# Performance work log

Measured on AMD Instinct MI355X. Metric: run time of the kernel, lower is better.

The kernel has to match this reference:

```python
import jax, jax.numpy as jnp
import numpy as np

DIM = 512; NH = 8; AG = 144; WIN = 18; PS = 12; B = 128; N0 = 320


def _pool_matrix(in_size, out_size):
    # PyTorch AdaptiveAvgPool2d window rule: start=floor(i*in/out), end=ceil((i+1)*in/out)
    P = np.zeros((out_size, in_size), np.float32)
    for i in range(out_size):
        s = (i * in_size) // out_size
        e = -((-(i + 1) * in_size) // out_size)
        P[i, s:e] = 1.0 / (e - s)
    return jnp.asarray(P)


def setup_inputs() -> dict:
    key = jax.random.key(0)
    ks = jax.random.split(key, 12)
    std = 0.02
    return {
        "x": jax.random.normal(ks[0], (B, N0, DIM), jnp.float32),
        "qkv_w": jax.random.normal(ks[1], (DIM, 3 * DIM), jnp.float32) * 0.02,
        "proj_w": jax.random.normal(ks[2], (DIM, DIM), jnp.float32) * 0.02,
        "proj_b": jnp.zeros((DIM,), jnp.float32),
        "dwc_w": jax.random.normal(ks[3], (DIM, 1, 3, 3), jnp.float32) * 0.1,
        "dwc_b": jnp.zeros((DIM,), jnp.float32),
        "an_bias": jax.random.normal(ks[4], (NH, AG, 7, 7), jnp.float32) * std,
        "na_bias": jax.random.normal(ks[5], (NH, AG, 7, 7), jnp.float32) * std,
        "ah_bias": jax.random.normal(ks[6], (1, NH, AG, WIN, 1), jnp.float32) * std,
        "aw_bias": jax.random.normal(ks[7], (1, NH, AG, 1, WIN), jnp.float32) * std,
        "ha_bias": jax.random.normal(ks[8], (1, NH, WIN, 1, AG), jnp.float32) * std,
        "wa_bias": jax.random.normal(ks[9], (1, NH, 1, WIN, AG), jnp.float32) * std,
    }


def reference(x, qkv_w, proj_w, proj_b, dwc_w, dwc_b,
              an_bias, na_bias, ah_bias, aw_bias, ha_bias, wa_bias):
    b, n0, c = x.shape
    x1 = jnp.pad(x, ((0, 0), (2, 2), (0, 0)))          # pad 2 tokens each side
    n = n0 + 4
    h = w = int(n ** 0.5)
    hd = c // NH
    scale = hd ** -0.5

    qkv = x1 @ qkv_w                                    # (b, n, 3c), no bias
    q, k, v = jnp.split(qkv, 3, axis=-1)

    # agent tokens: adaptive avg pool of q on the (h, w) grid to (PS, PS)
    P = _pool_matrix(h, PS)                             # (12, 18)
    qg = q.reshape(b, h, w, c)
    agent = jnp.einsum('oh,bhwc,pw->bopc', P, qg, P).reshape(b, AG, c)

    def heads(t):
        return t.reshape(b, n, NH, hd).transpose(0, 2, 1, 3)
    q, k, v = heads(q), heads(k), heads(v)              # (b, H, n, hd)
    ag = agent.reshape(b, AG, NH, hd).transpose(0, 2, 1, 3)  # (b, H, A, hd)

    # stage 1: agent <- keys  (ac_bias is concatenated then sliced off => no-op)
    pb1 = jax.image.resize(an_bias, (NH, AG, WIN, WIN), 'bilinear').reshape(1, NH, AG, WIN * WIN)
    pb2 = (ah_bias + aw_bias).reshape(1, NH, AG, WIN * WIN)
    agent_attn = jax.nn.softmax(
        jnp.einsum('bhad,bhnd->bhan', ag * scale, k) + pb1 + pb2, axis=-1)
    agent_v = jnp.einsum('bhan,bhnd->bhad', agent_attn, v)   # (b, H, A, hd)

    # stage 2: queries <- agents (ca_bias sliced off => no-op)
    ab1 = jax.image.resize(na_bias, (NH, AG, WIN, WIN), 'bilinear') \
        .reshape(1, NH, AG, WIN * WIN).transpose(0, 1, 3, 2)  # (1, H, n, A)
    ab2 = (ha_bias + wa_bias).reshape(1, NH, WIN * WIN, AG)
    q_attn = jax.nn.softmax(
        jnp.einsum('bhnd,bhad->bhna', q * scale, ag) + ab1 + ab2, axis=-1)
    out = jnp.einsum('bhna,bhad->bhnd', q_attn, agent_v)
    out = out.transpose(0, 2, 1, 3).reshape(b, n, c)

    # depthwise conv skip on v
    vimg = v.transpose(0, 2, 1, 3).reshape(b, h, w, c).transpose(0, 3, 1, 2)  # (b, c, h, w)
    dwc = jax.lax.conv_general_dilated(vimg, dwc_w, (1, 1), 'SAME',
                                       feature_group_count=c)
    dwc = dwc + dwc_b[None, :, None, None]
    out = out + dwc.transpose(0, 2, 3, 1).reshape(b, n, c)

    out = out @ proj_w + proj_b
    return out[:, 2:-2, :]
```

## Files before the change

kernel.cpp:

```cpp
#include <hip/hip_runtime.h>

typedef unsigned short u16;
typedef short bf16x8 __attribute__((ext_vector_type(8)));
typedef float f32x4 __attribute__((ext_vector_type(4)));

#define B_    128
#define N0_   320
#define C_    512
#define NH_   8
#define HD_   64
#define NTOK  324
#define H_    18
#define AG_   144
#define SCALE 0.125f

typedef __attribute__((address_space(3))) unsigned int as3_u32;
typedef __attribute__((address_space(1))) const unsigned int as1_u32;

__device__ __forceinline__ void gl_lds16(const void* g, void* l) {
  __builtin_amdgcn_global_load_lds((as1_u32*)(unsigned long long)g,
                                   (as3_u32*)(unsigned int)(unsigned long long)l,
                                   16, 0, 0);
}

__device__ __forceinline__ float bfu2f(u16 u) {
  union { unsigned int u; float f; } v; v.u = ((unsigned int)u) << 16; return v.f;
}
__device__ __forceinline__ u16 f2bfu(float f) {
  union { float f; unsigned int u; } v; v.f = f;
  unsigned int r = v.u + 0x7fffu + ((v.u >> 16) & 1u);
  return (u16)(r >> 16);
}

__global__ __launch_bounds__(256) void conv_x(const float* __restrict__ x, u16* __restrict__ xp)
{
  const int idx = blockIdx.x * 256 + threadIdx.x;
  const int row = idx >> 6, c8 = idx & 63;
  const int b = row / NTOK, t = row - b * NTOK;
  u16 o[8];
  if (t < 2 || t >= 322) {
    #pragma unroll
    for (int j = 0; j < 8; ++j) o[j] = 0;
  } else {
    const float* src = x + ((size_t)(b * N0_ + (t - 2))) * C_ + c8 * 8;
    const float4 f0 = *(const float4*)(src);
    const float4 f1 = *(const float4*)(src + 4);
    o[0]=f2bfu(f0.x); o[1]=f2bfu(f0.y); o[2]=f2bfu(f0.z); o[3]=f2bfu(f0.w);
    o[4]=f2bfu(f1.x); o[5]=f2bfu(f1.y); o[6]=f2bfu(f1.z); o[7]=f2bfu(f1.w);
  }
  *(bf16x8*)&xp[(size_t)row * C_ + c8 * 8] = *(bf16x8*)o;
}

__global__ __launch_bounds__(256) void tconv(const float* __restrict__ W, u16* __restrict__ Wt, int ncols)
{
  __shared__ float T[64][65];
  const int k0 = blockIdx.x * 64, n0 = blockIdx.y * 64;
  const int tid = threadIdx.x;
  const int rr = tid >> 4, cc = tid & 15;
  #pragma unroll
  for (int i = 0; i < 4; ++i) {
    const float4 f = *(const float4*)&W[(size_t)(k0 + i * 16 + rr) * ncols + n0 + cc * 4];
    T[i * 16 + rr][cc * 4 + 0] = f.x; T[i * 16 + rr][cc * 4 + 1] = f.y;
    T[i * 16 + rr][cc * 4 + 2] = f.z; T[i * 16 + rr][cc * 4 + 3] = f.w;
  }
  __syncthreads();
  #pragma unroll
  for (int i = 0; i < 4; ++i) {
    const int n = i * 16 + rr;
    ushort4 u;
    u.x = f2bfu(T[cc * 4 + 0][n]); u.y = f2bfu(T[cc * 4 + 1][n]);
    u.z = f2bfu(T[cc * 4 + 2][n]); u.w = f2bfu(T[cc * 4 + 3][n]);
    *(ushort4*)&Wt[(size_t)(n0 + n) * 512 + k0 + cc * 4] = u;
  }
}

template<int MODE>
__global__ __launch_bounds__(256) void mfma_gemm(
    const u16* __restrict__ A, const u16* __restrict__ Bt,
    u16* __restrict__ qb, u16* __restrict__ kb, u16* __restrict__ vb,
    const float* __restrict__ bias, float* __restrict__ outf)
{
  __shared__ __align__(16) u16 As[128 * 64];
  __shared__ __align__(16) u16 Bs[128 * 64];
  const int bx = blockIdx.x;
  const int by = blockIdx.y;
  const int tid = threadIdx.x;
  const int wv = tid >> 6, lane = tid & 63;
  const int lr = lane & 15, lk = lane >> 4;
  const int wr = wv >> 1, wc = wv & 1;
  const int si = lane >> 3, slot = lane & 7;

  size_t arow_src[4];
  #pragma unroll
  for (int jj = 0; jj < 4; ++jj) {
    const int rl = (wv * 4 + jj) * 8 + si;
    const int r = by * 128 + rl;
    if (MODE == 0) {
      arow_src[jj] = (size_t)r * 512;
    } else {
      const int b2 = r / N0_, ii = r - b2 * N0_;
      arow_src[jj] = ((size_t)b2 * 8 * NTOK + (ii + 2)) * 64;
    }
  }

  f32x4 acc[4][4] = {};
  for (int k0 = 0; k0 < 512; k0 += 64) {
    __syncthreads();
    #pragma unroll
    for (int jj = 0; jj < 4; ++jj) {
      const int rl = (wv * 4 + jj) * 8 + si;
      const int c = slot ^ (rl & 7);
      const u16* asrc = (MODE == 0)
          ? (A + arow_src[jj] + k0 + c * 8)
          : (A + arow_src[jj] + (size_t)(k0 >> 6) * (NTOK * 64) + c * 8);
      gl_lds16(asrc, (char*)As + (wv * 4 + jj) * 1024);
      gl_lds16(Bt + (size_t)(bx * 128 + rl) * 512 + k0 + c * 8,
               (char*)Bs + (wv * 4 + jj) * 1024);
    }
    __syncthreads();
    #pragma unroll
    for (int kk = 0; kk < 2; ++kk) {
      bf16x8 af[4], bf[4];
      #pragma unroll
      for (int m = 0; m < 4; ++m) {
        const int row = wr * 64 + m * 16 + lr;
        af[m] = *(const bf16x8*)((const char*)As + row * 128 + (((kk * 4 + lk) ^ (row & 7)) << 4));
      }
      #pragma unroll
      for (int n = 0; n < 4; ++n) {
        const int row = wc * 64 + n * 16 + lr;
        bf[n] = *(const bf16x8*)((const char*)Bs + row * 128 + (((kk * 4 + lk) ^ (row & 7)) << 4));
      }
      #pragma unroll
      for (int m = 0; m < 4; ++m)
        #pragma unroll
        for (int n = 0; n < 4; ++n)
          acc[m][n] = __builtin_amdgcn_mfma_f32_16x16x32_bf16(af[m], bf[n], acc[m][n], 0, 0, 0);
    }
  }

  if (MODE == 0) {
    const int mat = (bx * 128) >> 9;
    u16* outp = (mat == 0) ? qb : (mat == 1) ? kb : vb;
    #pragma unroll
    for (int m = 0; m < 4; ++m) {
      #pragma unroll
      for (int r = 0; r < 4; ++r) {
        const int row = by * 128 + wr * 64 + m * 16 + lk * 4 + r;
        const int b = row / NTOK, t = row - b * NTOK;
        #pragma unroll
        for (int n = 0; n < 4; ++n) {
          const int col = bx * 128 + wc * 64 + n * 16 + lr;
          const int rem = col & 511, h = rem >> 6, d = rem & 63;
          outp[(((size_t)(b * NH_ + h)) * NTOK + t) * HD_ + d] = f2bfu(acc[m][n][r]);
        }
      }
    }
  } else {
    #pragma unroll
    for (int m = 0; m < 4; ++m) {
      #pragma unroll
      for (int r = 0; r < 4; ++r) {
        const int row = by * 128 + wr * 64 + m * 16 + lk * 4 + r;
        #pragma unroll
        for (int n = 0; n < 4; ++n) {
          const int col = bx * 128 + wc * 64 + n * 16 + lr;
          outf[(size_t)row * C_ + col] = acc[m][n][r] + bias[col];
        }
      }
    }
  }
}

__global__ void bias_kernel(const float* __restrict__ an, const float* __restrict__ na,
                            const float* __restrict__ ah, const float* __restrict__ aw,
                            const float* __restrict__ ha, const float* __restrict__ wa,
                            float* __restrict__ bAN, float* __restrict__ bNA)
{
  const int blk = blockIdx.x;
  const int h = blk / AG_, a = blk - h * AG_;
  const int tid = threadIdx.x;
  if (tid >= NTOK) return;
  const int y = tid / H_, x = tid - y * H_;
  float cy = (y + 0.5f) * (7.0f / 18.0f) - 0.5f; cy = fminf(fmaxf(cy, 0.f), 6.f);
  float cx = (x + 0.5f) * (7.0f / 18.0f) - 0.5f; cx = fminf(fmaxf(cx, 0.f), 6.f);
  const int y0 = (int)floorf(cy); const float ty = cy - y0; const int y1 = min(y0 + 1, 6);
  const int x0 = (int)floorf(cx); const float tx = cx - x0; const int x1 = min(x0 + 1, 6);
  const float w00 = (1.f - ty) * (1.f - tx), w01 = (1.f - ty) * tx;
  const float w10 = ty * (1.f - tx), w11 = ty * tx;
  const float* anp = an + (size_t)blk * 49;
  const float* nap = na + (size_t)blk * 49;
  const float van = w00 * anp[y0*7+x0] + w01 * anp[y0*7+x1] + w10 * anp[y1*7+x0] + w11 * anp[y1*7+x1];
  const float vna = w00 * nap[y0*7+x0] + w01 * nap[y0*7+x1] + w10 * nap[y1*7+x0] + w11 * nap[y1*7+x1];
  bAN[(size_t)blk * NTOK + tid] = van + ah[(size_t)blk * H_ + y] + aw[(size_t)blk * H_ + x];
  bNA[((size_t)h * NTOK + tid) * AG_ + a] =
      vna + ha[((size_t)h * H_ + y) * AG_ + a] + wa[((size_t)h * H_ + x) * AG_ + a];
}

__global__ __launch_bounds__(512) void pool_kernel(const u16* __restrict__ qb, u16* __restrict__ agb)
{
  const int blk = blockIdx.x;
  const int b = blk / AG_, a = blk - b * AG_;
  const int o = a / 12, pc = a - o * 12;
  const int y0 = (3 * o) >> 1, x0 = (3 * pc) >> 1;
  const int c = threadIdx.x; const int h = c >> 6, d = c & 63;
  const size_t base = ((size_t)(b * NH_ + h)) * NTOK * HD_ + d;
  const int t00 = (y0 * H_ + x0) * HD_;
  const float v = bfu2f(qb[base + t00]) + bfu2f(qb[base + t00 + HD_])
                + bfu2f(qb[base + t00 + H_ * HD_]) + bfu2f(qb[base + t00 + H_ * HD_ + HD_]);
  agb[((size_t)(b * NH_ + h)) * AG_ * HD_ + a * HD_ + d] = f2bfu(0.25f * v);
}

__global__ __launch_bounds__(576) void fused_attn(
    const u16* __restrict__ kb, const u16* __restrict__ vb,
    const u16* __restrict__ qb, const u16* __restrict__ agb,
    const float* __restrict__ bAN, const float* __restrict__ bNA,
    const float* __restrict__ dwc_w, const float* __restrict__ dwc_b,
    u16* __restrict__ aob)
{
  __shared__ __align__(16) u16 vT[64 * 360];
  __shared__ __align__(16) u16 avT[64 * 168];
  __shared__ __align__(16) u16 pW[9][16][40];
  const int bh = blockIdx.x, h = bh & 7;
  const int tid = threadIdx.x;
  const int mt = tid >> 6;
  const int l = tid & 63, lr = l & 15, lk = l >> 4;

  for (int idx = tid; idx < 128; idx += 576)
    *(bf16x8*)&avT[(idx >> 1) * 168 + 144 + (idx & 1) * 8] = (bf16x8){0,0,0,0,0,0,0,0};

  const u16* vsrc = vb + (size_t)bh * NTOK * HD_;
  for (int idx = tid; idx < 64 * 45; idx += 576) {
    const int d = idx & 63, c = idx >> 6;
    bf16x8 tv;
    #pragma unroll
    for (int j = 0; j < 8; ++j) {
      const int n = c * 8 + j;
      tv[j] = (n < NTOK) ? (short)vsrc[(size_t)n * HD_ + d] : (short)0;
    }
    *(bf16x8*)&vT[d * 360 + c * 8] = tv;
  }

  const u16* aga = agb + ((size_t)bh * AG_ + mt * 16 + lr) * HD_ + lk * 8;
  const bf16x8 a0 = *(const bf16x8*)(aga);
  const bf16x8 a1 = *(const bf16x8*)(aga + 32);

  f32x4 acc[21];
  const u16* kbase = kb + (size_t)bh * NTOK * HD_ + lk * 8;
  #pragma unroll
  for (int nt = 0; nt < 21; ++nt) {
    const bf16x8 b0 = *(const bf16x8*)(kbase + (size_t)(nt * 16 + lr) * HD_);
    const bf16x8 b1 = *(const bf16x8*)(kbase + (size_t)(nt * 16 + lr) * HD_ + 32);
    f32x4 c = {0.f, 0.f, 0.f, 0.f};
    c = __builtin_amdgcn_mfma_f32_16x16x32_bf16(a0, b0, c, 0, 0, 0);
    c = __builtin_amdgcn_mfma_f32_16x16x32_bf16(a1, b1, c, 0, 0, 0);
    acc[nt] = c;
  }

  const float* bb = bAN + ((size_t)h * AG_ + mt * 16) * NTOK;
  float mx[4] = {-1e30f, -1e30f, -1e30f, -1e30f};
  #pragma unroll
  for (int nt = 0; nt < 21; ++nt) {
    const int col = nt * 16 + lr;
    const bool valid = (nt < 20) || (lr < 4);
    #pragma unroll
    for (int r = 0; r < 4; ++r) {
      float s = -1e30f;
      if (valid) s = acc[nt][r] * SCALE + bb[(lk * 4 + r) * NTOK + col];
      acc[nt][r] = s;
      mx[r] = fmaxf(mx[r], s);
    }
  }
  #pragma unroll
  for (int r = 0; r < 4; ++r) {
    #pragma unroll
    for (int o = 1; o < 16; o <<= 1) mx[r] = fmaxf(mx[r], __shfl_xor(mx[r], o));
  }
  float sm[4] = {0.f, 0.f, 0.f, 0.f};
  #pragma unroll
  for (int nt = 0; nt < 21; ++nt) {
    #pragma unroll
    for (int r = 0; r < 4; ++r) {
      const float e = __expf(acc[nt][r] - mx[r]);
      acc[nt][r] = e;
      sm[r] += e;
    }
  }
  #pragma unroll
  for (int r = 0; r < 4; ++r) {
    #pragma unroll
    for (int o = 1; o < 16; o <<= 1) sm[r] += __shfl_xor(sm[r], o);
    sm[r] = 1.0f / sm[r];
  }

  __syncthreads();

  f32x4 ov[4];
  #pragma unroll
  for (int nt2 = 0; nt2 < 4; ++nt2) ov[nt2] = (f32x4){0.f, 0.f, 0.f, 0.f};
  for (int ks = 0; ks < 11; ++ks) {
    #pragma unroll
    for (int half = 0; half < 2; ++half) {
      const int nt = 2 * ks + half;
      #pragma unroll
      for (int r = 0; r < 4; ++r)
        pW[mt][lk * 4 + r][half * 16 + lr] = (nt < 21) ? f2bfu(acc[nt][r] * sm[r]) : (u16)0;
    }
    const bf16x8 pa = *(const bf16x8*)&pW[mt][lr][lk * 8];
    #pragma unroll
    for (int nt2 = 0; nt2 < 4; ++nt2) {
      const bf16x8 vf = *(const bf16x8*)&vT[(nt2 * 16 + lr) * 360 + ks * 32 + lk * 8];
      ov[nt2] = __builtin_amdgcn_mfma_f32_16x16x32_bf16(pa, vf, ov[nt2], 0, 0, 0);
    }
  }
  #pragma unroll
  for (int nt2 = 0; nt2 < 4; ++nt2) {
    ushort4 u;
    u.x = f2bfu(ov[nt2][0]); u.y = f2bfu(ov[nt2][1]);
    u.z = f2bfu(ov[nt2][2]); u.w = f2bfu(ov[nt2][3]);
    *(ushort4*)&avT[(nt2 * 16 + lr) * 168 + mt * 16 + lk * 4] = u;
  }

  __syncthreads();

  u16* aout = aob + (size_t)bh * NTOK * HD_;
  for (int mt2 = mt; mt2 < 21; mt2 += 9) {
    const int arow = min(mt2 * 16 + lr, NTOK - 1);
    const u16* qa = qb + ((size_t)bh * NTOK + arow) * HD_ + lk * 8;
    const bf16x8 qa0 = *(const bf16x8*)(qa);
    const bf16x8 qa1 = *(const bf16x8*)(qa + 32);

    f32x4 acc2[9];
    #pragma unroll
    for (int nt = 0; nt < 9; ++nt) {
      const u16* bp = agb + ((size_t)bh * AG_ + nt * 16 + lr) * HD_ + lk * 8;
      f32x4 c = {0.f, 0.f, 0.f, 0.f};
      c = __builtin_amdgcn_mfma_f32_16x16x32_bf16(qa0, *(const bf16x8*)(bp), c, 0, 0, 0);
      c = __builtin_amdgcn_mfma_f32_16x16x32_bf16(qa1, *(const bf16x8*)(bp + 32), c, 0, 0, 0);
      acc2[nt] = c;
    }

    float mx2[4] = {-1e30f, -1e30f, -1e30f, -1e30f};
    #pragma unroll
    for (int nt = 0; nt < 9; ++nt) {
      #pragma unroll
      for (int r = 0; r < 4; ++r) {
        const int trow = min(mt2 * 16 + lk * 4 + r, NTOK - 1);
        const float s = acc2[nt][r] * SCALE + bNA[((size_t)h * NTOK + trow) * AG_ + nt * 16 + lr];
        acc2[nt][r] = s;
        mx2[r] = fmaxf(mx2[r], s);
      }
    }
    #pragma unroll
    for (int r = 0; r < 4; ++r) {
      #pragma unroll
      for (int o = 1; o < 16; o <<= 1) mx2[r] = fmaxf(mx2[r], __shfl_xor(mx2[r], o));
    }
    float sm2[4] = {0.f, 0.f, 0.f, 0.f};
    #pragma unroll
    for (int nt = 0; nt < 9; ++nt) {
      #pragma unroll
      for (int r = 0; r < 4; ++r) {
        const float e = __expf(acc2[nt][r] - mx2[r]);
        acc2[nt][r] = e;
        sm2[r] += e;
      }
    }
    #pragma unroll
    for (int r = 0; r < 4; ++r) {
      #pragma unroll
      for (int o = 1; o < 16; o <<= 1) sm2[r] += __shfl_xor(sm2[r], o);
      sm2[r] = 1.0f / sm2[r];
    }

    f32x4 ov2[4];
    #pragma unroll
    for (int nt2 = 0; nt2 < 4; ++nt2) ov2[nt2] = (f32x4){0.f, 0.f, 0.f, 0.f};
    for (int ks = 0; ks < 5; ++ks) {
      #pragma unroll
      for (int half = 0; half < 2; ++half) {
        const int nt = 2 * ks + half;
        #pragma unroll
        for (int r = 0; r < 4; ++r)
          pW[mt][lk * 4 + r][half * 16 + lr] = (nt < 9) ? f2bfu(acc2[nt][r] * sm2[r]) : (u16)0;
      }
      const bf16x8 pa = *(const bf16x8*)&pW[mt][lr][lk * 8];
      #pragma unroll
      for (int nt2 = 0; nt2 < 4; ++nt2) {
        const bf16x8 vf = *(const bf16x8*)&avT[(nt2 * 16 + lr) * 168 + ks * 32 + lk * 8];
        ov2[nt2] = __builtin_amdgcn_mfma_f32_16x16x32_bf16(pa, vf, ov2[nt2], 0, 0, 0);
      }
    }

    #pragma unroll
    for (int nt2 = 0; nt2 < 4; ++nt2) {
      const int d = nt2 * 16 + lr;
      const float* wp = dwc_w + (size_t)(h * 64 + d) * 9;
      float w9[9];
      #pragma unroll
      for (int j = 0; j < 9; ++j) w9[j] = wp[j];
      const float cb = dwc_b[h * 64 + d];
      #pragma unroll
      for (int r = 0; r < 4; ++r) {
        const int t = mt2 * 16 + lk * 4 + r;
        if (t < NTOK) {
          const int y = t / H_, x = t - y * H_;
          float conv = cb;
          #pragma unroll
          for (int ky = 0; ky < 3; ++ky) {
            const int yy = y + ky - 1;
            if (yy < 0 || yy >= H_) continue;
            #pragma unroll
            for (int kx = 0; kx < 3; ++kx) {
              const int xc = x + kx - 1;
              if (xc < 0 || xc >= H_) continue;
              conv += w9[ky * 3 + kx] * bfu2f(vT[d * 360 + yy * H_ + xc]);
            }
          }
          aout[(size_t)t * HD_ + d] = f2bfu(ov2[nt2][r] + conv);
        }
      }
    }
  }
}

extern "C" void kernel_launch(void* const* d_in, const int* in_sizes, int n_in,
                              void* d_out, int out_size, void* d_ws, size_t ws_size,
                              hipStream_t stream)
{
  (void)in_sizes; (void)n_in; (void)out_size;
  const float* x      = (const float*)d_in[0];
  const float* qkv_w  = (const float*)d_in[1];
  const float* proj_w = (const float*)d_in[2];
  const float* proj_b = (const float*)d_in[3];
  const float* dwc_w  = (const float*)d_in[4];
  const float* dwc_b  = (const float*)d_in[5];
  const float* an     = (const float*)d_in[6];
  const float* na     = (const float*)d_in[7];
  const float* ah     = (const float*)d_in[8];
  const float* aw     = (const float*)d_in[9];
  const float* ha     = (const float*)d_in[10];
  const float* wa     = (const float*)d_in[11];

  char* ws = (char*)d_ws;
  const size_t QB  = (size_t)B_ * NH_ * NTOK * HD_ * 2;
  const size_t AGB = (size_t)B_ * NH_ * AG_  * HD_ * 2;
  const size_t BB  = (size_t)NH_ * AG_ * NTOK * 4;
  const size_t WQ  = (size_t)1536 * 512 * 2;
  const size_t WP  = (size_t)512 * 512 * 2;
  u16* qb    = (u16*)(ws);
  u16* kb    = (u16*)(ws + QB);
  u16* vb    = (u16*)(ws + 2 * QB);
  u16* xp    = (u16*)(ws + 3 * QB);
  u16* agb   = (u16*)(ws + 3 * QB);
  float* bAN = (float*)(ws + 3 * QB + AGB);
  float* bNA = (float*)(ws + 3 * QB + AGB + BB);
  u16* wqkvT = (u16*)(ws + 4 * QB);
  u16* wprojT= (u16*)(ws + 4 * QB + WQ);
  u16* aob   = kb;
  if (ws_size < 4 * QB + WQ + WP) return;

  conv_x   <<<dim3(B_ * NTOK * 64 / 256), dim3(256), 0, stream>>>(x, xp);
  tconv    <<<dim3(8, 24), dim3(256), 0, stream>>>(qkv_w, wqkvT, 1536);
  tconv    <<<dim3(8, 8),  dim3(256), 0, stream>>>(proj_w, wprojT, 512);
  mfma_gemm<0><<<dim3(12, 324), dim3(256), 0, stream>>>(xp, wqkvT, qb, kb, vb, nullptr, nullptr);
  pool_kernel<<<dim3(B_ * AG_),  dim3(512), 0, stream>>>(qb, agb);
  bias_kernel<<<dim3(NH_ * AG_), dim3(324), 0, stream>>>(an, na, ah, aw, ha, wa, bAN, bNA);
  fused_attn<<<dim3(B_ * NH_), dim3(576), 0, stream>>>(kb, vb, qb, agb, bAN, bNA, dwc_w, dwc_b, aob);
  mfma_gemm<1><<<dim3(4, 320), dim3(256), 0, stream>>>(aob, wprojT, nullptr, nullptr, nullptr, proj_b, (float*)d_out);
}
```

Measured before the change: 526.8 us.

## Store attention biases in bf16, stage dwc weights in LDS, vectorize output stores

Position-bias tables are stored as bf16 instead of fp32, halving the bias traffic read by the fused attention kernel. The depthwise-conv weights and bias are staged once per block into LDS as bf16 instead of being reloaded from global memory per tile. The second-stage PV MFMA swaps operands so each lane holds four consecutive channels of one token, which allows ushort4 vectorized output stores. It also wraps the MFMA loops with s_setprio, and rounding the biases and conv weights to bf16 slightly lowers accuracy.

```diff
diff --git a/kernel.cpp b/kernel.cpp
--- a/kernel.cpp
+++ b/kernel.cpp
@@ -175,7 +175,7 @@
 __global__ void bias_kernel(const float* __restrict__ an, const float* __restrict__ na,
                             const float* __restrict__ ah, const float* __restrict__ aw,
                             const float* __restrict__ ha, const float* __restrict__ wa,
-                            float* __restrict__ bAN, float* __restrict__ bNA)
+                            u16* __restrict__ bAN, u16* __restrict__ bNA)
 {
   const int blk = blockIdx.x;
   const int h = blk / AG_, a = blk - h * AG_;
@@ -192,9 +192,9 @@
   const float* nap = na + (size_t)blk * 49;
   const float van = w00 * anp[y0*7+x0] + w01 * anp[y0*7+x1] + w10 * anp[y1*7+x0] + w11 * anp[y1*7+x1];
   const float vna = w00 * nap[y0*7+x0] + w01 * nap[y0*7+x1] + w10 * nap[y1*7+x0] + w11 * nap[y1*7+x1];
-  bAN[(size_t)blk * NTOK + tid] = van + ah[(size_t)blk * H_ + y] + aw[(size_t)blk * H_ + x];
+  bAN[(size_t)blk * NTOK + tid] = f2bfu(van + ah[(size_t)blk * H_ + y] + aw[(size_t)blk * H_ + x]);
   bNA[((size_t)h * NTOK + tid) * AG_ + a] =
-      vna + ha[((size_t)h * H_ + y) * AG_ + a] + wa[((size_t)h * H_ + x) * AG_ + a];
+      f2bfu(vna + ha[((size_t)h * H_ + y) * AG_ + a] + wa[((size_t)h * H_ + x) * AG_ + a]);
 }
 
 __global__ __launch_bounds__(512) void pool_kernel(const u16* __restrict__ qb, u16* __restrict__ agb)
@@ -214,18 +214,23 @@
 __global__ __launch_bounds__(576) void fused_attn(
     const u16* __restrict__ kb, const u16* __restrict__ vb,
     const u16* __restrict__ qb, const u16* __restrict__ agb,
-    const float* __restrict__ bAN, const float* __restrict__ bNA,
+    const u16* __restrict__ bAN, const u16* __restrict__ bNA,
     const float* __restrict__ dwc_w, const float* __restrict__ dwc_b,
     u16* __restrict__ aob)
 {
   __shared__ __align__(16) u16 vT[64 * 360];
   __shared__ __align__(16) u16 avT[64 * 168];
   __shared__ __align__(16) u16 pW[9][16][40];
+  __shared__ u16 wL[64 * 10];
   const int bh = blockIdx.x, h = bh & 7;
   const int tid = threadIdx.x;
   const int mt = tid >> 6;
   const int l = tid & 63, lr = l & 15, lk = l >> 4;
 
+  for (int idx = tid; idx < 640; idx += 576) {
+    const int d = idx / 10, j = idx - d * 10;
+    wL[idx] = f2bfu((j < 9) ? dwc_w[(size_t)(h * 64 + d) * 9 + j] : dwc_b[h * 64 + d]);
+  }
   for (int idx = tid; idx < 128; idx += 576)
     *(bf16x8*)&avT[(idx >> 1) * 168 + 144 + (idx & 1) * 8] = (bf16x8){0,0,0,0,0,0,0,0};
 
@@ -247,6 +252,7 @@
 
   f32x4 acc[21];
   const u16* kbase = kb + (size_t)bh * NTOK * HD_ + lk * 8;
+  __builtin_amdgcn_s_setprio(1);
   #pragma unroll
   for (int nt = 0; nt < 21; ++nt) {
     const bf16x8 b0 = *(const bf16x8*)(kbase + (size_t)(nt * 16 + lr) * HD_);
@@ -256,8 +262,9 @@
     c = __builtin_amdgcn_mfma_f32_16x16x32_bf16(a1, b1, c, 0, 0, 0);
     acc[nt] = c;
   }
-
-  const float* bb = bAN + ((size_t)h * AG_ + mt * 16) * NTOK;
+  __builtin_amdgcn_s_setprio(0);
+
+  const u16* bb = bAN + ((size_t)h * AG_ + mt * 16) * NTOK;
   float mx[4] = {-1e30f, -1e30f, -1e30f, -1e30f};
   #pragma unroll
   for (int nt = 0; nt < 21; ++nt) {
@@ -266,7 +273,7 @@
     #pragma unroll
     for (int r = 0; r < 4; ++r) {
       float s = -1e30f;
-      if (valid) s = acc[nt][r] * SCALE + bb[(lk * 4 + r) * NTOK + col];
+      if (valid) s = acc[nt][r] * SCALE + bfu2f(bb[(lk * 4 + r) * NTOK + col]);
       acc[nt][r] = s;
       mx[r] = fmaxf(mx[r], s);
     }
@@ -307,11 +314,13 @@
         pW[mt][lk * 4 + r][half * 16 + lr] = (nt < 21) ? f2bfu(acc[nt][r] * sm[r]) : (u16)0;
     }
     const bf16x8 pa = *(const bf16x8*)&pW[mt][lr][lk * 8];
+    __builtin_amdgcn_s_setprio(1);
     #pragma unroll
     for (int nt2 = 0; nt2 < 4; ++nt2) {
       const bf16x8 vf = *(const bf16x8*)&vT[(nt2 * 16 + lr) * 360 + ks * 32 + lk * 8];
       ov[nt2] = __builtin_amdgcn_mfma_f32_16x16x32_bf16(pa, vf, ov[nt2], 0, 0, 0);
     }
+    __builtin_amdgcn_s_setprio(0);
   }
   #pragma unroll
   for (int nt2 = 0; nt2 < 4; ++nt2) {
@@ -331,6 +340,7 @@
     const bf16x8 qa1 = *(const bf16x8*)(qa + 32);
 
     f32x4 acc2[9];
+    __builtin_amdgcn_s_setprio(1);
     #pragma unroll
     for (int nt = 0; nt < 9; ++nt) {
       const u16* bp = agb + ((size_t)bh * AG_ + nt * 16 + lr) * HD_ + lk * 8;
@@ -339,6 +349,7 @@
       c = __builtin_amdgcn_mfma_f32_16x16x32_bf16(qa1, *(const bf16x8*)(bp + 32), c, 0, 0, 0);
       acc2[nt] = c;
     }
+    __builtin_amdgcn_s_setprio(0);
 
     float mx2[4] = {-1e30f, -1e30f, -1e30f, -1e30f};
     #pragma unroll
@@ -346,7 +357,7 @@
       #pragma unroll
       for (int r = 0; r < 4; ++r) {
         const int trow = min(mt2 * 16 + lk * 4 + r, NTOK - 1);
-        const float s = acc2[nt][r] * SCALE + bNA[((size_t)h * NTOK + trow) * AG_ + nt * 16 + lr];
+        const float s = acc2[nt][r] * SCALE + bfu2f(bNA[((size_t)h * NTOK + trow) * AG_ + nt * 16 + lr]);
         acc2[nt][r] = s;
         mx2[r] = fmaxf(mx2[r], s);
       }
@@ -375,7 +386,7 @@
 
     f32x4 ov2[4];
     #pragma unroll
-    for (int nt2 = 0; nt2 < 4; ++nt2) ov2[nt2] = (f32x4){0.f, 0.f, 0.f, 0.f};
+    for (int dt = 0; dt < 4; ++dt) ov2[dt] = (f32x4){0.f, 0.f, 0.f, 0.f};
     for (int ks = 0; ks < 5; ++ks) {
       #pragma unroll
       for (int half = 0; half < 2; ++half) {
@@ -385,27 +396,25 @@
           pW[mt][lk * 4 + r][half * 16 + lr] = (nt < 9) ? f2bfu(acc2[nt][r] * sm2[r]) : (u16)0;
       }
       const bf16x8 pa = *(const bf16x8*)&pW[mt][lr][lk * 8];
-      #pragma unroll
-      for (int nt2 = 0; nt2 < 4; ++nt2) {
-        const bf16x8 vf = *(const bf16x8*)&avT[(nt2 * 16 + lr) * 168 + ks * 32 + lk * 8];
-        ov2[nt2] = __builtin_amdgcn_mfma_f32_16x16x32_bf16(pa, vf, ov2[nt2], 0, 0, 0);
-      }
-    }
-
-    #pragma unroll
-    for (int nt2 = 0; nt2 < 4; ++nt2) {
-      const int d = nt2 * 16 + lr;
-      const float* wp = dwc_w + (size_t)(h * 64 + d) * 9;
-      float w9[9];
-      #pragma unroll
-      for (int j = 0; j < 9; ++j) w9[j] = wp[j];
-      const float cb = dwc_b[h * 64 + d];
-      #pragma unroll
-      for (int r = 0; r < 4; ++r) {
-        const int t = mt2 * 16 + lk * 4 + r;
-        if (t < NTOK) {
-          const int y = t / H_, x = t - y * H_;
-          float conv = cb;
+      __builtin_amdgcn_s_setprio(1);
+      #pragma unroll
+      for (int dt = 0; dt < 4; ++dt) {
+        const bf16x8 vf = *(const bf16x8*)&avT[(dt * 16 + lr) * 168 + ks * 32 + lk * 8];
+        ov2[dt] = __builtin_amdgcn_mfma_f32_16x16x32_bf16(vf, pa, ov2[dt], 0, 0, 0);
+      }
+      __builtin_amdgcn_s_setprio(0);
+    }
+
+    const int t = mt2 * 16 + lr;
+    if (t < NTOK) {
+      const int y = t / H_, x = t - y * H_;
+      #pragma unroll
+      for (int dt = 0; dt < 4; ++dt) {
+        ushort4 u;
+        #pragma unroll
+        for (int r = 0; r < 4; ++r) {
+          const int d = dt * 16 + lk * 4 + r;
+          float conv = bfu2f(wL[d * 10 + 9]);
           #pragma unroll
           for (int ky = 0; ky < 3; ++ky) {
             const int yy = y + ky - 1;
@@ -414,11 +423,12 @@
             for (int kx = 0; kx < 3; ++kx) {
               const int xc = x + kx - 1;
               if (xc < 0 || xc >= H_) continue;
-              conv += w9[ky * 3 + kx] * bfu2f(vT[d * 360 + yy * H_ + xc]);
+              conv += bfu2f(wL[d * 10 + ky * 3 + kx]) * bfu2f(vT[d * 360 + yy * H_ + xc]);
             }
           }
-          aout[(size_t)t * HD_ + d] = f2bfu(ov2[nt2][r] + conv);
+          ((u16*)&u)[r] = f2bfu(ov2[dt][r] + conv);
         }
+        *(ushort4*)&aout[(size_t)t * HD_ + dt * 16 + lk * 4] = u;
       }
     }
   }
@@ -445,7 +455,7 @@
   char* ws = (char*)d_ws;
   const size_t QB  = (size_t)B_ * NH_ * NTOK * HD_ * 2;
   const size_t AGB = (size_t)B_ * NH_ * AG_  * HD_ * 2;
-  const size_t BB  = (size_t)NH_ * AG_ * NTOK * 4;
+  const size_t BB  = (size_t)NH_ * AG_ * NTOK * 2;
   const size_t WQ  = (size_t)1536 * 512 * 2;
   const size_t WP  = (size_t)512 * 512 * 2;
   u16* qb    = (u16*)(ws);
@@ -453,8 +463,8 @@
   u16* vb    = (u16*)(ws + 2 * QB);
   u16* xp    = (u16*)(ws + 3 * QB);
   u16* agb   = (u16*)(ws + 3 * QB);
-  float* bAN = (float*)(ws + 3 * QB + AGB);
-  float* bNA = (float*)(ws + 3 * QB + AGB + BB);
+  u16* bAN   = (u16*)(ws + 3 * QB + AGB);
+  u16* bNA   = (u16*)(ws + 3 * QB + AGB + BB);
   u16* wqkvT = (u16*)(ws + 4 * QB);
   u16* wprojT= (u16*)(ws + 4 * QB + WQ);
   u16* aob   = kb;
```

Result: faster. 502.0 us (-4.7%).
